# Optimization experiments

Measured on AMD Instinct MI355X. Metric: run time of the kernel, lower is better.

## Reference

```python
import jax, jax.numpy as jnp
import numpy as np

N_NODES = 100000


def setup_inputs() -> dict:
    key = jax.random.key(0)
    ks = jax.random.split(key, 8)
    nfeat, hdim, nclass, E = 512, 64, 256, 3200000
    x = jax.random.normal(ks[0], (N_NODES, nfeat), dtype=jnp.float32)
    edge_index = jax.random.randint(ks[1], (2, E), 0, N_NODES, dtype=jnp.int64)
    Win = jax.random.normal(ks[2], (nfeat, hdim), dtype=jnp.float32) * (1.0 / np.sqrt(nfeat))
    b_in = jnp.zeros((hdim,), dtype=jnp.float32)
    Wl = jax.random.normal(ks[3], (4, hdim, hdim), dtype=jnp.float32) * (1.0 / np.sqrt(hdim))
    bl = jnp.zeros((4, hdim), dtype=jnp.float32)
    Wr = jax.random.normal(ks[4], (4, hdim, hdim), dtype=jnp.float32) * (1.0 / np.sqrt(hdim))
    Wout = jax.random.normal(ks[5], (hdim, nclass), dtype=jnp.float32) * (1.0 / np.sqrt(hdim))
    b_out = jnp.zeros((nclass,), dtype=jnp.float32)
    return {"x": x, "edge_index": edge_index, "Win": Win, "b_in": b_in,
            "Wl": Wl, "bl": bl, "Wr": Wr, "Wout": Wout, "b_out": b_out}


def reference(x, edge_index, Win, b_in, Wl, bl, Wr, Wout, b_out):
    src, dst = edge_index[0], edge_index[1]
    # in-degree counts for scatter-mean (clamped to >=1 as in PyG)
    cnt = jax.ops.segment_sum(jnp.ones((src.shape[0],), dtype=x.dtype), dst,
                              num_segments=N_NODES)
    inv_cnt = (1.0 / jnp.maximum(cnt, 1.0))[:, None]  # [N,1]

    h = x @ Win + b_in  # [N, 64]
    for i in range(4):
        msg = h[src]  # gather neighbor features [E, 64]
        agg = jax.ops.segment_sum(msg, dst, num_segments=N_NODES) * inv_cnt
        conv = agg @ Wl[i] + bl[i] + h @ Wr[i]  # SAGEConv: lin_l(agg) + lin_r(h)
        h = h + jax.nn.relu(conv)  # residual
    return h @ Wout + b_out
```

## Files before the change

kernel.cpp:

```cpp
#include <hip/hip_runtime.h>
#include <hip/hip_bf16.h>

#define NN 100000
#define EE 3200000
#define HD 64
#define NF 512
#define NC 256

#define BSH 8
#define NB 391
#define EB 8192
#define NEB 391


__global__ __launch_bounds__(256) void part_count(const int* __restrict__ dst, int* __restrict__ hist) {
    __shared__ int hs[NB];
    int t = threadIdx.x, blk = blockIdx.x;
    for (int b = t; b < NB; b += 256) hs[b] = 0;
    __syncthreads();
    int base = blk * EB;
#pragma unroll
    for (int i = 0; i < EB / 256; ++i) {
        int e = base + t + 256 * i;
        if (e < EE) atomicAdd(&hs[dst[e] >> BSH], 1);
    }
    __syncthreads();
    for (int b = t; b < NB; b += 256) hist[blk * NB + b] = hs[b];
}


__global__ __launch_bounds__(512) void bucket_ptr(const int* __restrict__ hist, int* __restrict__ bucketptr) {
    __shared__ int s[512];
    int t = threadIdx.x;
    int v = 0;
    if (t < NB) {
        for (int blk = 0; blk < NEB; ++blk) v += hist[blk * NB + t];
    }
    s[t] = v; __syncthreads();
    for (int d = 1; d < 512; d <<= 1) {
        int a = (t >= d) ? s[t - d] : 0;
        __syncthreads();
        s[t] += a;
        __syncthreads();
    }
    if (t < NB) bucketptr[t] = s[t] - v;
    if (t == 0) bucketptr[NB] = EE;
}


__global__ __launch_bounds__(512) void part_scan(const int* __restrict__ hist, const int* __restrict__ bucketptr,
                                                 int* __restrict__ bboff) {
    __shared__ int s[512];
    int b = blockIdx.x, t = threadIdx.x;
    int v = (t < NEB) ? hist[t * NB + b] : 0;
    s[t] = v; __syncthreads();
    for (int d = 1; d < 512; d <<= 1) {
        int a = (t >= d) ? s[t - d] : 0;
        __syncthreads();
        s[t] += a;
        __syncthreads();
    }
    if (t < NEB) bboff[t * NB + b] = bucketptr[b] + s[t] - v;
}


__global__ __launch_bounds__(256) void part_scatter(const int* __restrict__ src, const int* __restrict__ dst,
                                                    const int* __restrict__ bboff, unsigned int* __restrict__ ebuf) {
    __shared__ int off[NB];
    __shared__ int rank[NB];
    int t = threadIdx.x, blk = blockIdx.x;
    for (int b = t; b < NB; b += 256) { off[b] = bboff[blk * NB + b]; rank[b] = 0; }
    __syncthreads();
    int base = blk * EB;
#pragma unroll
    for (int i = 0; i < EB / 256; ++i) {
        int e = base + t + 256 * i;
        if (e < EE) {
            int d = dst[e];
            int s = src[e];
            int b = d >> BSH;
            int r = atomicAdd(&rank[b], 1);
            ebuf[off[b] + r] = (unsigned)s | ((unsigned)(d & 255) << 17);
        }
    }
}


__global__ __launch_bounds__(256) void bucket_fill2(const unsigned int* __restrict__ ebuf,
                                                    const int* __restrict__ bucketptr,
                                                    int* __restrict__ rowptr, float* __restrict__ inv,
                                                    int* __restrict__ csr) {
    __shared__ int hcnt[256];
    __shared__ int scn[256];
    __shared__ int cur[256];
    int t = threadIdx.x, b = blockIdx.x;
    int n0 = b << BSH;
    hcnt[t] = 0;
    __syncthreads();
    int estart = bucketptr[b];
    int eend = bucketptr[b + 1];
    for (int e = estart + t; e < eend; e += 256) {
        atomicAdd(&hcnt[ebuf[e] >> 17], 1);
    }
    __syncthreads();
    int v = hcnt[t];
    scn[t] = v;
    __syncthreads();
    for (int d = 1; d < 256; d <<= 1) {
        int a = (t >= d) ? scn[t - d] : 0;
        __syncthreads();
        scn[t] += a;
        __syncthreads();
    }
    int off = estart + scn[t] - v;
    cur[t] = off;
    if (n0 + t < NN) {
        rowptr[n0 + t] = off;
        inv[n0 + t] = 1.0f / (float)(v > 1 ? v : 1);
    }
    if (b == NB - 1 && t == 0) rowptr[NN] = EE;
    __syncthreads();
    for (int e = estart + t; e < eend; e += 256) {
        unsigned u = ebuf[e];
        int dL = (int)(u >> 17);
        int p = atomicAdd(&cur[dL], 1);
        csr[p] = (int)(u & 0x1FFFFu);
    }
}


__global__ __launch_bounds__(256) void gemm_in(const float* __restrict__ x, const float* __restrict__ Win,
                                               const float* __restrict__ b_in, float* __restrict__ h) {
    __shared__ float xs[128 * 64];
    __shared__ float ws[64 * 64];
    int tid = threadIdx.x;
    int cg = tid & 15;
    int rg = tid >> 4;
    int rowBase = blockIdx.x * 128;
    float4 bb = *(const float4*)(b_in + cg * 4);
    float acc[8][4];
#pragma unroll
    for (int r = 0; r < 8; ++r) {
        acc[r][0] = bb.x; acc[r][1] = bb.y; acc[r][2] = bb.z; acc[r][3] = bb.w;
    }

    for (int kt = 0; kt < NF; kt += 64) {
        __syncthreads();
#pragma unroll
        for (int i = 0; i < 8; ++i) {
            int idx = tid + 256 * i;
            int r = idx >> 4;
            int c4 = idx & 15;
            int grow = rowBase + r;
            if (grow >= NN) grow = NN - 1;
            int c4s = c4 ^ ((r >> 3) & 3);
            *(float4*)(xs + r * 64 + c4s * 4) = *(const float4*)(x + (size_t)grow * NF + kt + c4 * 4);
        }
#pragma unroll
        for (int i = 0; i < 4; ++i) {
            int idx = tid + 256 * i;
            int r = idx >> 4;
            int c4 = idx & 15;
            *(float4*)(ws + r * 64 + c4 * 4) = *(const float4*)(Win + (size_t)(kt + r) * HD + c4 * 4);
        }
        __syncthreads();
#pragma unroll 2
        for (int k = 0; k < 64; k += 4) {
            int kq = k >> 2;
            float4 w0 = *(const float4*)(ws + (k + 0) * 64 + cg * 4);
            float4 w1 = *(const float4*)(ws + (k + 1) * 64 + cg * 4);
            float4 w2 = *(const float4*)(ws + (k + 2) * 64 + cg * 4);
            float4 w3 = *(const float4*)(ws + (k + 3) * 64 + cg * 4);
#pragma unroll
            for (int r = 0; r < 8; ++r) {
                int row = rg * 8 + r;
                int c4s = kq ^ ((row >> 3) & 3);
                float4 xv = *(const float4*)(xs + row * 64 + c4s * 4);
                acc[r][0] = fmaf(xv.x, w0.x, acc[r][0]);
                acc[r][1] = fmaf(xv.x, w0.y, acc[r][1]);
                acc[r][2] = fmaf(xv.x, w0.z, acc[r][2]);
                acc[r][3] = fmaf(xv.x, w0.w, acc[r][3]);
                acc[r][0] = fmaf(xv.y, w1.x, acc[r][0]);
                acc[r][1] = fmaf(xv.y, w1.y, acc[r][1]);
                acc[r][2] = fmaf(xv.y, w1.z, acc[r][2]);
                acc[r][3] = fmaf(xv.y, w1.w, acc[r][3]);
                acc[r][0] = fmaf(xv.z, w2.x, acc[r][0]);
                acc[r][1] = fmaf(xv.z, w2.y, acc[r][1]);
                acc[r][2] = fmaf(xv.z, w2.z, acc[r][2]);
                acc[r][3] = fmaf(xv.z, w2.w, acc[r][3]);
                acc[r][0] = fmaf(xv.w, w3.x, acc[r][0]);
                acc[r][1] = fmaf(xv.w, w3.y, acc[r][1]);
                acc[r][2] = fmaf(xv.w, w3.z, acc[r][2]);
                acc[r][3] = fmaf(xv.w, w3.w, acc[r][3]);
            }
        }
    }
#pragma unroll
    for (int r = 0; r < 8; ++r) {
        int row = rowBase + rg * 8 + r;
        if (row < NN) {
            float4 o;
            o.x = acc[r][0]; o.y = acc[r][1]; o.z = acc[r][2]; o.w = acc[r][3];
            *(float4*)(h + (size_t)row * HD + cg * 4) = o;
        }
    }
}


__global__ __launch_bounds__(256) void aggregate(const float4* __restrict__ h4, const int* __restrict__ rowptr,
                                                 const int* __restrict__ csr, const float* __restrict__ inv,
                                                 float4* __restrict__ agg4) {
    int tid = threadIdx.x;
    int lane = tid & 63;
    int q = lane >> 4;
    int f = lane & 15;
    int node = blockIdx.x * 4 + (tid >> 6);
    int n = __builtin_amdgcn_readfirstlane(node);
    int start = rowptr[n];
    int end = rowptr[n + 1];

    float4 acc0 = make_float4(0.f, 0.f, 0.f, 0.f);
    float4 acc1 = make_float4(0.f, 0.f, 0.f, 0.f);
    int e = start;
    int end8 = start + ((end - start) & ~7);
    for (; e < end8; e += 8) {
        int s0 = csr[e + q];
        int s1 = csr[e + 4 + q];
        float4 v0 = h4[(size_t)s0 * 16 + f];
        float4 v1 = h4[(size_t)s1 * 16 + f];
        acc0.x += v0.x; acc0.y += v0.y; acc0.z += v0.z; acc0.w += v0.w;
        acc1.x += v1.x; acc1.y += v1.y; acc1.z += v1.z; acc1.w += v1.w;
    }
    if (e + q < end) {
        int s = csr[e + q];
        float4 v = h4[(size_t)s * 16 + f];
        acc0.x += v.x; acc0.y += v.y; acc0.z += v.z; acc0.w += v.w;
    }
    e += 4;
    if (e + q < end) {
        int s = csr[e + q];
        float4 v = h4[(size_t)s * 16 + f];
        acc1.x += v.x; acc1.y += v.y; acc1.z += v.z; acc1.w += v.w;
    }

    float4 a;
    a.x = acc0.x + acc1.x;
    a.y = acc0.y + acc1.y;
    a.z = acc0.z + acc1.z;
    a.w = acc0.w + acc1.w;
    a.x += __shfl_xor(a.x, 16); a.x += __shfl_xor(a.x, 32);
    a.y += __shfl_xor(a.y, 16); a.y += __shfl_xor(a.y, 32);
    a.z += __shfl_xor(a.z, 16); a.z += __shfl_xor(a.z, 32);
    a.w += __shfl_xor(a.w, 16); a.w += __shfl_xor(a.w, 32);

    if (q == 0) {
        float s = inv[n];
        float4 r;
        r.x = a.x * s; r.y = a.y * s; r.z = a.z * s; r.w = a.w * s;
        agg4[(size_t)n * 16 + f] = r;
    }
}


__global__ __launch_bounds__(256) void layer_conv(const float* __restrict__ agg, float* __restrict__ h,
                                                  const float* __restrict__ Wl, const float* __restrict__ Wr,
                                                  const float* __restrict__ bl) {
    __shared__ float as_[64 * 64];
    __shared__ float hs[64 * 64];
    int tid = threadIdx.x;
    int cg = tid & 15;
    int rg = tid >> 4;
    int rowBase = blockIdx.x * 64;
    float4 bb = *(const float4*)(bl + cg * 4);
    float acc[4][4];
#pragma unroll
    for (int r = 0; r < 4; ++r) {
        acc[r][0] = bb.x; acc[r][1] = bb.y; acc[r][2] = bb.z; acc[r][3] = bb.w;
    }

#pragma unroll
    for (int i = 0; i < 4; ++i) {
        int idx = tid + 256 * i;
        int r = idx >> 4;
        int c4 = idx & 15;
        int grow = rowBase + r;
        if (grow >= NN) grow = NN - 1;
        int c4s = c4 ^ ((r >> 2) & 3);
        *(float4*)(as_ + r * 64 + c4s * 4) = *(const float4*)(agg + (size_t)grow * HD + c4 * 4);
        *(float4*)(hs + r * 64 + c4s * 4) = *(const float4*)(h + (size_t)grow * HD + c4 * 4);
    }
    __syncthreads();

#pragma unroll 2
    for (int k = 0; k < 64; k += 4) {
        int kq = k >> 2;
        float4 l0 = *(const float4*)(Wl + (size_t)(k + 0) * HD + cg * 4);
        float4 l1 = *(const float4*)(Wl + (size_t)(k + 1) * HD + cg * 4);
        float4 l2 = *(const float4*)(Wl + (size_t)(k + 2) * HD + cg * 4);
        float4 l3 = *(const float4*)(Wl + (size_t)(k + 3) * HD + cg * 4);
        float4 r0 = *(const float4*)(Wr + (size_t)(k + 0) * HD + cg * 4);
        float4 r1 = *(const float4*)(Wr + (size_t)(k + 1) * HD + cg * 4);
        float4 r2 = *(const float4*)(Wr + (size_t)(k + 2) * HD + cg * 4);
        float4 r3 = *(const float4*)(Wr + (size_t)(k + 3) * HD + cg * 4);
#pragma unroll
        for (int r = 0; r < 4; ++r) {
            int row = rg * 4 + r;
            int c4s = kq ^ ((row >> 2) & 3);
            float4 av = *(const float4*)(as_ + row * 64 + c4s * 4);
            float4 hv = *(const float4*)(hs + row * 64 + c4s * 4);
            acc[r][0] = fmaf(av.x, l0.x, acc[r][0]);
            acc[r][1] = fmaf(av.x, l0.y, acc[r][1]);
            acc[r][2] = fmaf(av.x, l0.z, acc[r][2]);
            acc[r][3] = fmaf(av.x, l0.w, acc[r][3]);
            acc[r][0] = fmaf(av.y, l1.x, acc[r][0]);
            acc[r][1] = fmaf(av.y, l1.y, acc[r][1]);
            acc[r][2] = fmaf(av.y, l1.z, acc[r][2]);
            acc[r][3] = fmaf(av.y, l1.w, acc[r][3]);
            acc[r][0] = fmaf(av.z, l2.x, acc[r][0]);
            acc[r][1] = fmaf(av.z, l2.y, acc[r][1]);
            acc[r][2] = fmaf(av.z, l2.z, acc[r][2]);
            acc[r][3] = fmaf(av.z, l2.w, acc[r][3]);
            acc[r][0] = fmaf(av.w, l3.x, acc[r][0]);
            acc[r][1] = fmaf(av.w, l3.y, acc[r][1]);
            acc[r][2] = fmaf(av.w, l3.z, acc[r][2]);
            acc[r][3] = fmaf(av.w, l3.w, acc[r][3]);
            acc[r][0] = fmaf(hv.x, r0.x, acc[r][0]);
            acc[r][1] = fmaf(hv.x, r0.y, acc[r][1]);
            acc[r][2] = fmaf(hv.x, r0.z, acc[r][2]);
            acc[r][3] = fmaf(hv.x, r0.w, acc[r][3]);
            acc[r][0] = fmaf(hv.y, r1.x, acc[r][0]);
            acc[r][1] = fmaf(hv.y, r1.y, acc[r][1]);
            acc[r][2] = fmaf(hv.y, r1.z, acc[r][2]);
            acc[r][3] = fmaf(hv.y, r1.w, acc[r][3]);
            acc[r][0] = fmaf(hv.z, r2.x, acc[r][0]);
            acc[r][1] = fmaf(hv.z, r2.y, acc[r][1]);
            acc[r][2] = fmaf(hv.z, r2.z, acc[r][2]);
            acc[r][3] = fmaf(hv.z, r2.w, acc[r][3]);
            acc[r][0] = fmaf(hv.w, r3.x, acc[r][0]);
            acc[r][1] = fmaf(hv.w, r3.y, acc[r][1]);
            acc[r][2] = fmaf(hv.w, r3.z, acc[r][2]);
            acc[r][3] = fmaf(hv.w, r3.w, acc[r][3]);
        }
    }

#pragma unroll
    for (int r = 0; r < 4; ++r) {
        int row = rowBase + rg * 4 + r;
        if (row < NN) {
            int lrow = rg * 4 + r;
            int c4s = cg ^ ((lrow >> 2) & 3);
            float4 ho = *(const float4*)(hs + lrow * 64 + c4s * 4);
            float4 o;
            float c0 = acc[r][0], c1 = acc[r][1], c2 = acc[r][2], c3 = acc[r][3];
            o.x = ho.x + (c0 > 0.f ? c0 : 0.f);
            o.y = ho.y + (c1 > 0.f ? c1 : 0.f);
            o.z = ho.z + (c2 > 0.f ? c2 : 0.f);
            o.w = ho.w + (c3 > 0.f ? c3 : 0.f);
            *(float4*)(h + (size_t)row * HD + cg * 4) = o;
        }
    }
}


__global__ __launch_bounds__(256) void gemm_out_k(const float* __restrict__ h, const float* __restrict__ Wout,
                                                  const float* __restrict__ b_out, float* __restrict__ out) {
    __shared__ float hs[32 * 64];
    int tid = threadIdx.x;
    int cg = tid & 63;
    int rg = tid >> 6;
    int rowBase = blockIdx.x * 32;
#pragma unroll
    for (int i = 0; i < 2; ++i) {
        int idx = tid + 256 * i;
        int r = idx >> 4;
        int c4 = idx & 15;
        int grow = rowBase + r;
        if (grow >= NN) grow = NN - 1;
        *(float4*)(hs + r * 64 + c4 * 4) = *(const float4*)(h + (size_t)grow * HD + c4 * 4);
    }
    __syncthreads();

    float4 bb = *(const float4*)(b_out + cg * 4);
    float acc[8][4];
#pragma unroll
    for (int r = 0; r < 8; ++r) {
        acc[r][0] = bb.x; acc[r][1] = bb.y; acc[r][2] = bb.z; acc[r][3] = bb.w;
    }

#pragma unroll 2
    for (int k = 0; k < 64; k += 4) {
        float4 w0 = *(const float4*)(Wout + (size_t)(k + 0) * NC + cg * 4);
        float4 w1 = *(const float4*)(Wout + (size_t)(k + 1) * NC + cg * 4);
        float4 w2 = *(const float4*)(Wout + (size_t)(k + 2) * NC + cg * 4);
        float4 w3 = *(const float4*)(Wout + (size_t)(k + 3) * NC + cg * 4);
#pragma unroll
        for (int r = 0; r < 8; ++r) {
            float4 hv = *(const float4*)(hs + (rg * 8 + r) * 64 + k);
            acc[r][0] = fmaf(hv.x, w0.x, acc[r][0]);
            acc[r][1] = fmaf(hv.x, w0.y, acc[r][1]);
            acc[r][2] = fmaf(hv.x, w0.z, acc[r][2]);
            acc[r][3] = fmaf(hv.x, w0.w, acc[r][3]);
            acc[r][0] = fmaf(hv.y, w1.x, acc[r][0]);
            acc[r][1] = fmaf(hv.y, w1.y, acc[r][1]);
            acc[r][2] = fmaf(hv.y, w1.z, acc[r][2]);
            acc[r][3] = fmaf(hv.y, w1.w, acc[r][3]);
            acc[r][0] = fmaf(hv.z, w2.x, acc[r][0]);
            acc[r][1] = fmaf(hv.z, w2.y, acc[r][1]);
            acc[r][2] = fmaf(hv.z, w2.z, acc[r][2]);
            acc[r][3] = fmaf(hv.z, w2.w, acc[r][3]);
            acc[r][0] = fmaf(hv.w, w3.x, acc[r][0]);
            acc[r][1] = fmaf(hv.w, w3.y, acc[r][1]);
            acc[r][2] = fmaf(hv.w, w3.z, acc[r][2]);
            acc[r][3] = fmaf(hv.w, w3.w, acc[r][3]);
        }
    }
#pragma unroll
    for (int r = 0; r < 8; ++r) {
        int row = rowBase + rg * 8 + r;
        if (row < NN) {
            float4 o;
            o.x = acc[r][0]; o.y = acc[r][1]; o.z = acc[r][2]; o.w = acc[r][3];
            *(float4*)(out + (size_t)row * NC + cg * 4) = o;
        }
    }
}

extern "C" void kernel_launch(void* const* d_in, const int* in_sizes, int n_in,
                              void* d_out, int out_size, void* d_ws, size_t ws_size,
                              hipStream_t stream) {
    const float* x    = (const float*)d_in[0];
    const int*   ei   = (const int*)d_in[1];
    const float* Win  = (const float*)d_in[2];
    const float* b_in = (const float*)d_in[3];
    const float* Wl   = (const float*)d_in[4];
    const float* bl   = (const float*)d_in[5];
    const float* Wr   = (const float*)d_in[6];
    const float* Wout = (const float*)d_in[7];
    const float* b_out= (const float*)d_in[8];
    float* out = (float*)d_out;

    const int* src = ei;
    const int* dst = ei + EE;

    char* ws = (char*)d_ws;
    float* h        = (float*)ws;
    float* agg      = h + (size_t)NN * HD;
    int*   rowptr   = (int*)(agg + (size_t)NN * HD);
    int*   csr      = rowptr + 100004;
    float* inv      = (float*)(csr + EE);
    int*   bucketptr= (int*)(inv + NN);

    unsigned int* ebuf = (unsigned int*)agg;
    int* hist  = (int*)agg + EE;
    int* bboff = hist + NEB * NB;

    part_count<<<NEB, 256, 0, stream>>>(dst, hist);
    bucket_ptr<<<1, 512, 0, stream>>>(hist, bucketptr);
    part_scan<<<NB, 512, 0, stream>>>(hist, bucketptr, bboff);
    part_scatter<<<NEB, 256, 0, stream>>>(src, dst, bboff, ebuf);
    bucket_fill2<<<NB, 256, 0, stream>>>(ebuf, bucketptr, rowptr, inv, csr);

    gemm_in<<<(NN + 127) / 128, 256, 0, stream>>>(x, Win, b_in, h);

    for (int i = 0; i < 4; ++i) {
        aggregate<<<NN / 4, 256, 0, stream>>>((const float4*)h, rowptr, csr, inv, (float4*)agg);
        layer_conv<<<(NN + 63) / 64, 256, 0, stream>>>(agg, h, Wl + (size_t)i * HD * HD,
                                                       Wr + (size_t)i * HD * HD, bl + (size_t)i * HD);
    }

    gemm_out_k<<<(NN + 31) / 32, 256, 0, stream>>>(h, Wout, b_out, out);
}
```

Before: 1.094 ms.

## Use bf16 MFMA for input projection GEMM with prepacked weights

Replaces the FP32 FMA-based x@Win kernel with a bf16 MFMA 16x16x32 implementation. x tiles are converted to bf16 while being loaded into swizzled shared memory, and Win is prepacked once by a new small kernel into an MFMA operand layout read directly from global memory. This cuts ALU work for the 100000x512x64 GEMM, which is likely bound by reading x from memory, at the cost of bf16 rounding of x and Win.

```diff
diff --git a/kernel.cpp b/kernel.cpp
--- a/kernel.cpp
+++ b/kernel.cpp
@@ -11,6 +11,17 @@
 #define NB 391
 #define EB 8192
 #define NEB 391
+
+typedef __attribute__((ext_vector_type(8))) short bf16x8;
+typedef __attribute__((ext_vector_type(4))) float f32x4;
+
+__device__ __forceinline__ unsigned short f2bf(float f) {
+    unsigned u = __float_as_uint(f);
+    return (unsigned short)((u + 0x7FFFu + ((u >> 16) & 1u)) >> 16);
+}
+__device__ __forceinline__ unsigned pack2(float a, float b) {
+    return (unsigned)f2bf(a) | ((unsigned)f2bf(b) << 16);
+}
 
 
 __global__ __launch_bounds__(256) void part_count(const int* __restrict__ dst, int* __restrict__ hist) {
@@ -129,79 +140,93 @@
 }
 
 
-__global__ __launch_bounds__(256) void gemm_in(const float* __restrict__ x, const float* __restrict__ Win,
+__global__ __launch_bounds__(256) void pack_w(const float* __restrict__ Win, unsigned short* __restrict__ wpk) {
+    int id = blockIdx.x * 256 + threadIdx.x;
+    int l = id & 63;
+    int c = (id >> 6) & 3;
+    int t = id >> 8;
+    int kbase = t * 32 + (l >> 4) * 8;
+    int col = c * 16 + (l & 15);
+    float f[8];
+#pragma unroll
+    for (int j = 0; j < 8; ++j) f[j] = Win[(size_t)(kbase + j) * HD + col];
+    uint4 p;
+    p.x = pack2(f[0], f[1]); p.y = pack2(f[2], f[3]);
+    p.z = pack2(f[4], f[5]); p.w = pack2(f[6], f[7]);
+    *(uint4*)(wpk + (size_t)id * 8) = p;
+}
+
+
+__global__ __launch_bounds__(256) void gemm_in(const float* __restrict__ x, const unsigned short* __restrict__ wpk,
                                                const float* __restrict__ b_in, float* __restrict__ h) {
-    __shared__ float xs[128 * 64];
-    __shared__ float ws[64 * 64];
+    __shared__ unsigned short xs[128 * 64];
     int tid = threadIdx.x;
-    int cg = tid & 15;
-    int rg = tid >> 4;
+    int lane = tid & 63;
+    int w = tid >> 6;
     int rowBase = blockIdx.x * 128;
-    float4 bb = *(const float4*)(b_in + cg * 4);
-    float acc[8][4];
-#pragma unroll
-    for (int r = 0; r < 8; ++r) {
-        acc[r][0] = bb.x; acc[r][1] = bb.y; acc[r][2] = bb.z; acc[r][3] = bb.w;
+    int lr = lane & 15;
+    int lg = lane >> 4;
+
+    f32x4 acc[2][4];
+#pragma unroll
+    for (int c = 0; c < 4; ++c) {
+        float bb = b_in[c * 16 + lr];
+#pragma unroll
+        for (int m = 0; m < 2; ++m) acc[m][c] = (f32x4){bb, bb, bb, bb};
     }
 
     for (int kt = 0; kt < NF; kt += 64) {
         __syncthreads();
 #pragma unroll
-        for (int i = 0; i < 8; ++i) {
+        for (int i = 0; i < 4; ++i) {
             int idx = tid + 256 * i;
-            int r = idx >> 4;
-            int c4 = idx & 15;
+            int r = idx >> 3;
+            int u = idx & 7;
             int grow = rowBase + r;
             if (grow >= NN) grow = NN - 1;
-            int c4s = c4 ^ ((r >> 3) & 3);
-            *(float4*)(xs + r * 64 + c4s * 4) = *(const float4*)(x + (size_t)grow * NF + kt + c4 * 4);
-        }
-#pragma unroll
-        for (int i = 0; i < 4; ++i) {
-            int idx = tid + 256 * i;
-            int r = idx >> 4;
-            int c4 = idx & 15;
-            *(float4*)(ws + r * 64 + c4 * 4) = *(const float4*)(Win + (size_t)(kt + r) * HD + c4 * 4);
-        }
-        __syncthreads();
-#pragma unroll 2
-        for (int k = 0; k < 64; k += 4) {
-            int kq = k >> 2;
-            float4 w0 = *(const float4*)(ws + (k + 0) * 64 + cg * 4);
-            float4 w1 = *(const float4*)(ws + (k + 1) * 64 + cg * 4);
-            float4 w2 = *(const float4*)(ws + (k + 2) * 64 + cg * 4);
-            float4 w3 = *(const float4*)(ws + (k + 3) * 64 + cg * 4);
-#pragma unroll
-            for (int r = 0; r < 8; ++r) {
-                int row = rg * 8 + r;
-                int c4s = kq ^ ((row >> 3) & 3);
-                float4 xv = *(const float4*)(xs + row * 64 + c4s * 4);
-                acc[r][0] = fmaf(xv.x, w0.x, acc[r][0]);
-                acc[r][1] = fmaf(xv.x, w0.y, acc[r][1]);
-                acc[r][2] = fmaf(xv.x, w0.z, acc[r][2]);
-                acc[r][3] = fmaf(xv.x, w0.w, acc[r][3]);
-                acc[r][0] = fmaf(xv.y, w1.x, acc[r][0]);
-                acc[r][1] = fmaf(xv.y, w1.y, acc[r][1]);
-                acc[r][2] = fmaf(xv.y, w1.z, acc[r][2]);
-                acc[r][3] = fmaf(xv.y, w1.w, acc[r][3]);
-                acc[r][0] = fmaf(xv.z, w2.x, acc[r][0]);
-                acc[r][1] = fmaf(xv.z, w2.y, acc[r][1]);
-                acc[r][2] = fmaf(xv.z, w2.z, acc[r][2]);
-                acc[r][3] = fmaf(xv.z, w2.w, acc[r][3]);
-                acc[r][0] = fmaf(xv.w, w3.x, acc[r][0]);
-                acc[r][1] = fmaf(xv.w, w3.y, acc[r][1]);
-                acc[r][2] = fmaf(xv.w, w3.z, acc[r][2]);
-                acc[r][3] = fmaf(xv.w, w3.w, acc[r][3]);
+            const float* srcp = x + (size_t)grow * NF + kt + u * 8;
+            float4 a = *(const float4*)(srcp);
+            float4 b = *(const float4*)(srcp + 4);
+            uint4 p;
+            p.x = pack2(a.x, a.y); p.y = pack2(a.z, a.w);
+            p.z = pack2(b.x, b.y); p.w = pack2(b.z, b.w);
+            int u2 = u ^ (r & 7);
+            *(uint4*)(xs + (size_t)r * 64 + u2 * 8) = p;
+        }
+        __syncthreads();
+#pragma unroll
+        for (int ks = 0; ks < 2; ++ks) {
+            int tstep = (kt >> 5) + ks;
+            bf16x8 av[2], bv[4];
+#pragma unroll
+            for (int m = 0; m < 2; ++m) {
+                int r = w * 32 + m * 16 + lr;
+                int u2 = (ks * 4 + lg) ^ (r & 7);
+                av[m] = *(const bf16x8*)(xs + (size_t)r * 64 + u2 * 8);
             }
-        }
-    }
-#pragma unroll
-    for (int r = 0; r < 8; ++r) {
-        int row = rowBase + rg * 8 + r;
-        if (row < NN) {
-            float4 o;
-            o.x = acc[r][0]; o.y = acc[r][1]; o.z = acc[r][2]; o.w = acc[r][3];
-            *(float4*)(h + (size_t)row * HD + cg * 4) = o;
+#pragma unroll
+            for (int c = 0; c < 4; ++c) {
+                bv[c] = *(const bf16x8*)(wpk + (((size_t)tstep * 4 + c) * 64 + lane) * 8);
+            }
+#pragma unroll
+            for (int m = 0; m < 2; ++m)
+#pragma unroll
+                for (int c = 0; c < 4; ++c)
+                    acc[m][c] = __builtin_amdgcn_mfma_f32_16x16x32_bf16(av[m], bv[c], acc[m][c], 0, 0, 0);
+        }
+    }
+
+#pragma unroll
+    for (int m = 0; m < 2; ++m) {
+        int rbase = rowBase + w * 32 + m * 16 + lg * 4;
+#pragma unroll
+        for (int j = 0; j < 4; ++j) {
+            int row = rbase + j;
+            if (row < NN) {
+#pragma unroll
+                for (int c = 0; c < 4; ++c)
+                    h[(size_t)row * HD + c * 16 + lr] = acc[m][c][j];
+            }
         }
     }
 }
@@ -449,10 +474,13 @@
     int*   csr      = rowptr + 100004;
     float* inv      = (float*)(csr + EE);
     int*   bucketptr= (int*)(inv + NN);
+    unsigned short* wpk = (unsigned short*)(bucketptr + 400);
 
     unsigned int* ebuf = (unsigned int*)agg;
     int* hist  = (int*)agg + EE;
     int* bboff = hist + NEB * NB;
+
+    pack_w<<<16, 256, 0, stream>>>(Win, wpk);
 
     part_count<<<NEB, 256, 0, stream>>>(dst, hist);
     bucket_ptr<<<1, 512, 0, stream>>>(hist, bucketptr);
@@ -460,7 +488,7 @@
     part_scatter<<<NEB, 256, 0, stream>>>(src, dst, bboff, ebuf);
     bucket_fill2<<<NB, 256, 0, stream>>>(ebuf, bucketptr, rowptr, inv, csr);
 
-    gemm_in<<<(NN + 127) / 128, 256, 0, stream>>>(x, Win, b_in, h);
+    gemm_in<<<(NN + 127) / 128, 256, 0, stream>>>(x, wpk, b_in, h);
 
     for (int i = 0; i < 4; ++i) {
         aggregate<<<NN / 4, 256, 0, stream>>>((const float4*)h, rowptr, csr, inv, (float4*)agg);
```

Result: faster. 1.043 ms (-4.7%).
